# Optimization experiments

Measured on AMD Instinct MI355X. Metric: run time of the kernel, lower is better.

## Reference

```python
import jax, jax.numpy as jnp
import numpy as np

EPS = 1e-5  # torch BatchNorm default


def setup_inputs() -> dict:
    key = jax.random.key(0)
    k1, k2, k3 = jax.random.split(key, 3)
    N, C, T, V, O = 64, 64, 300, 25, 64
    x = jax.random.normal(k1, (N, C, T, V), dtype=jnp.float32)
    # 24 = V-1 convs, each (O, C, 1, 2) -> packed as (V-1, O, C, 2), scaled like conv_init
    W = jax.random.normal(k2, (V - 1, O, C, 2), dtype=jnp.float32) * (1.0 / np.sqrt(2 * C))
    b = jax.random.normal(k3, (V - 1, O), dtype=jnp.float32) * 0.01
    gamma = jnp.ones((O,), dtype=jnp.float32)
    beta = jnp.zeros((O,), dtype=jnp.float32)
    return {"x": x, "W": W, "b": b, "gamma": gamma, "beta": beta}


def reference(x, W, b, gamma, beta):
    # x: (N, C, T, V); W: (V-1, O, C, 2); b: (V-1, O)
    # Math of the original loop: out[..., v] = sum_i W0_i @ x[..., v]
    #   + sum_i W1_i @ x[..., (v+i+1) % V] + sum_i b_i
    V = x.shape[-1]
    W0 = W[..., 0]  # (V-1, O, C)
    W1 = W[..., 1]  # (V-1, O, C)
    # identity-tap term: all W0 share the same column -> sum once
    S0 = W0.sum(axis=0)  # (O, C)
    out = jnp.einsum('oc,nctv->notv', S0, x)
    # circular term: source u = (v+i+1)%V  <=>  i = (u-v-1)%V, valid for u != v
    v_idx = jnp.arange(V)
    off = (v_idx[None, :] - v_idx[:, None] - 1) % V  # (V_target, V_source) -> i, equals V-1 when u==v
    W1p = jnp.concatenate([W1, jnp.zeros_like(W1[:1])], axis=0)  # index V-1 maps to zero (u==v excluded)
    Wg = W1p[off]  # (V, V, O, C), zero on the diagonal
    out = out + jnp.einsum('vuoc,nctu->notv', Wg, x)
    out = out + b.sum(axis=0)[None, :, None, None]
    # BatchNorm2d (training-mode batch stats, biased variance) + ReLU
    mean = out.mean(axis=(0, 2, 3), keepdims=True)
    var = out.var(axis=(0, 2, 3), keepdims=True)
    out = (out - mean) * jax.lax.rsqrt(var + EPS)
    out = out * gamma[None, :, None, None] + beta[None, :, None, None]
    return jax.nn.relu(out)
```

## Files before the change

kernel.cpp:

```cpp
#include <hip/hip_runtime.h>


typedef short  s16x8 __attribute__((ext_vector_type(8)));
typedef float  f32x4 __attribute__((ext_vector_type(4)));

#define T_      300
#define TB_     19
#define NTHR_   320
#define ASTRIDE 136
#define TSTR    404

__device__ __forceinline__ unsigned short f2bf(float f) {
  unsigned u = __builtin_bit_cast(unsigned, f);
  return (unsigned short)((u + 0x7FFFu + ((u >> 16) & 1u)) >> 16);
}

__global__ void pack_w_kernel(const float* __restrict__ W, s16x8* __restrict__ Wg) {
  int idx = blockIdx.x * 256 + threadIdx.x;
  if (idx >= 12800) return;
  int lane  = idx & 63;
  int ni    = (idx >> 6) & 3;
  int chunk = (idx >> 8) & 1;
  int s     = idx >> 9;
  int o     = (ni << 4) + (lane & 15);
  int cbase = (chunk << 5) + ((lane >> 4) << 3);
  s16x8 h;
#pragma unroll
  for (int j = 0; j < 8; ++j) {
    int c = cbase + j;
    float val;
    if (s == 0) {
      val = 0.f;
      for (int i = 0; i < 24; ++i) val += W[((i * 64 + o) * 64 + c) * 2];
    } else {
      val = W[(((s - 1) * 64 + o) * 64 + c) * 2 + 1];
    }
    h[j] = (short)f2bf(val);
  }
  Wg[idx] = h;
}

__global__ __launch_bounds__(NTHR_) void tap_mm_kernel(
    const float* __restrict__ x, const s16x8* __restrict__ Wg,
    float* __restrict__ out, float* __restrict__ partials) {
  __shared__ __align__(16) char Ash[54400];
  __shared__ float red2[640];
  int n  = blockIdx.x;
  int tb = blockIdx.y;
  int t0 = tb * 16;
  int validRows = min(16, T_ - t0) * 25;
  int tid = threadIdx.x;
  const float* xn = x + n * 480000 + t0 * 25;

#pragma unroll 5
  for (int it = 0; it < 10; ++it) {
    int id  = tid + it * NTHR_;
    int pos = id % 400;
    int g   = id / 400;
    bool vld = pos < validRows;
    s16x8 h;
#pragma unroll
    for (int j = 0; j < 8; ++j) {
      float f = vld ? xn[((g << 3) + j) * 7500 + pos] : 0.f;
      h[j] = (short)f2bf(f);
    }
    *(s16x8*)(Ash + pos * ASTRIDE + (g << 4)) = h;
  }

  int wid = tid >> 6, lane = tid & 63;
  int l15 = lane & 15, lk = lane >> 4;
  int u[5], ao[5];
#pragma unroll
  for (int r = 0; r < 5; ++r) {
    int orow = ((wid * 5 + r) << 4) + l15;
    int tL = orow / 25;
    u[r]  = orow - tL * 25;
    ao[r] = orow * ASTRIDE + (lk << 4);
  }
  f32x4 acc[5][4];
#pragma unroll
  for (int r = 0; r < 5; ++r)
#pragma unroll
    for (int ct = 0; ct < 4; ++ct) acc[r][ct] = (f32x4){0.f, 0.f, 0.f, 0.f};

  s16x8 bf0[4], bf1[4];
#pragma unroll
  for (int ni = 0; ni < 4; ++ni) bf0[ni] = Wg[(ni << 6) + lane];
#pragma unroll
  for (int ni = 0; ni < 4; ++ni) bf1[ni] = Wg[256 + (ni << 6) + lane];

  __syncthreads();

  s16x8 afc = *(const s16x8*)(Ash + ao[0]);

  for (int s = 0; s < 25; ++s) {
    int snx = (s == 24) ? 0 : s + 1;
    const s16x8* wq0 = Wg + ((snx << 1) << 8);
    const s16x8* wq1 = wq0 + 256;
    __builtin_amdgcn_s_setprio(1);
#pragma unroll
    for (int r = 0; r < 5; ++r) {
      s16x8 nx = *(const s16x8*)(Ash + ((r < 4) ? ao[r + 1] : ao[0] + 64));
      acc[r][0] = __builtin_amdgcn_mfma_f32_16x16x32_bf16(afc, bf0[0], acc[r][0], 0, 0, 0);
      acc[r][1] = __builtin_amdgcn_mfma_f32_16x16x32_bf16(afc, bf0[1], acc[r][1], 0, 0, 0);
      acc[r][2] = __builtin_amdgcn_mfma_f32_16x16x32_bf16(afc, bf0[2], acc[r][2], 0, 0, 0);
      acc[r][3] = __builtin_amdgcn_mfma_f32_16x16x32_bf16(afc, bf0[3], acc[r][3], 0, 0, 0);
      afc = nx;
    }
    __builtin_amdgcn_s_setprio(0);
#pragma unroll
    for (int ni = 0; ni < 4; ++ni) bf0[ni] = wq0[(ni << 6) + lane];
    __builtin_amdgcn_s_setprio(1);
#pragma unroll
    for (int r = 0; r < 5; ++r) {
      int na;
      if (r < 4) {
        na = ao[r + 1] + 64;
      } else {
#pragma unroll
        for (int rr = 0; rr < 5; ++rr) {
          bool w = (u[rr] == 24);
          u[rr]  = w ? 0 : u[rr] + 1;
          ao[rr] += w ? -(24 * ASTRIDE) : ASTRIDE;
        }
        na = ao[0];
      }
      s16x8 nx = *(const s16x8*)(Ash + na);
      acc[r][0] = __builtin_amdgcn_mfma_f32_16x16x32_bf16(afc, bf1[0], acc[r][0], 0, 0, 0);
      acc[r][1] = __builtin_amdgcn_mfma_f32_16x16x32_bf16(afc, bf1[1], acc[r][1], 0, 0, 0);
      acc[r][2] = __builtin_amdgcn_mfma_f32_16x16x32_bf16(afc, bf1[2], acc[r][2], 0, 0, 0);
      acc[r][3] = __builtin_amdgcn_mfma_f32_16x16x32_bf16(afc, bf1[3], acc[r][3], 0, 0, 0);
      afc = nx;
    }
    __builtin_amdgcn_s_setprio(0);
#pragma unroll
    for (int ni = 0; ni < 4; ++ni) bf1[ni] = wq1[(ni << 6) + lane];
  }

  float s1v[4] = {0.f, 0.f, 0.f, 0.f}, s2v[4] = {0.f, 0.f, 0.f, 0.f};
#pragma unroll
  for (int r = 0; r < 5; ++r) {
#pragma unroll
    for (int qq = 0; qq < 4; ++qq) {
      int orow = ((wid * 5 + r) << 4) + (lk << 2) + qq;
      if (orow < validRows) {
#pragma unroll
        for (int ct = 0; ct < 4; ++ct) {
          float val = acc[r][ct][qq];
          s1v[ct] += val;
          s2v[ct] += val * val;
        }
      }
    }
  }
#pragma unroll
  for (int ct = 0; ct < 4; ++ct) {
    float a = s1v[ct], b = s2v[ct];
    a += __shfl_xor(a, 16); a += __shfl_xor(a, 32);
    b += __shfl_xor(b, 16); b += __shfl_xor(b, 32);
    if (lane < 16) {
      int base = ((((wid << 2) + ct) << 4) + l15) * 2;
      red2[base]     = a;
      red2[base + 1] = b;
    }
  }

  float* T = (float*)Ash;
  float* outb = out + n * 480000 + tb * 400;
  for (int qt = 0; qt < 4; ++qt) {
    __syncthreads();
#pragma unroll
    for (int r = 0; r < 5; ++r) {
      int row0 = wid * 80 + r * 16 + (lk << 2);
      *(f32x4*)&T[l15 * TSTR + row0] = acc[r][qt];
    }
    __syncthreads();
    if (qt == 0 && tid < 128) {
      int o = tid >> 1, m = tid & 1;
      int ct = o >> 4, ol = o & 15;
      float sres = 0.f;
#pragma unroll
      for (int w = 0; w < 5; ++w) sres += red2[((((w << 2) + ct) << 4) + ol) * 2 + m];
      int bl = blockIdx.y * 64 + blockIdx.x;
      partials[bl * 128 + m * 64 + o] = sres;
    }
#pragma unroll
    for (int i = 0; i < 5; ++i) {
      int idx = tid + i * 320;
      int ol  = idx / 100;
      int r4  = idx - ol * 100;
      if ((r4 << 2) < validRows) {
        float4 v = *(float4*)&T[ol * TSTR + (r4 << 2)];
        *(float4*)&outb[((qt << 4) + ol) * 7500 + (r4 << 2)] = v;
      }
    }
  }
}

__global__ void finalize_kernel(const float* __restrict__ part,
                                const float* __restrict__ gamma,
                                const float* __restrict__ beta,
                                float* __restrict__ scsh) {
  __shared__ float sm[512];
  int o = blockIdx.x;
  int tid = threadIdx.x;
  float s1 = 0.f, s2 = 0.f;
  for (int b = tid; b < 1216; b += 256) {
    s1 += part[b * 128 + o];
    s2 += part[b * 128 + 64 + o];
  }
  sm[tid] = s1; sm[256 + tid] = s2;
  __syncthreads();
  for (int st = 128; st >= 1; st >>= 1) {
    if (tid < st) { sm[tid] += sm[tid + st]; sm[256 + tid] += sm[256 + tid + st]; }
    __syncthreads();
  }
  if (tid == 0) {
    const float inv = 1.0f / 480000.0f;
    float mean = sm[0] * inv;
    float var  = sm[256] * inv - mean * mean;
    float sc = gamma[o] * rsqrtf(var + 1e-5f);
    float sh = beta[o] - mean * sc;
    scsh[o]      = sc;
    scsh[64 + o] = sh;
  }
}

__global__ void bn_relu_kernel(float4* __restrict__ out, const float* __restrict__ scsh) {
  int i = blockIdx.x * blockDim.x + threadIdx.x;
  const int total = 7680000;
  int stride = gridDim.x * blockDim.x;
  for (; i < total; i += stride) {
    int o = (i / 1875) & 63;
    float sc = scsh[o], sh = scsh[64 + o];
    float4 v = out[i];
    v.x = fmaxf(fmaf(v.x, sc, sh), 0.f);
    v.y = fmaxf(fmaf(v.y, sc, sh), 0.f);
    v.z = fmaxf(fmaf(v.z, sc, sh), 0.f);
    v.w = fmaxf(fmaf(v.w, sc, sh), 0.f);
    out[i] = v;
  }
}

extern "C" void kernel_launch(void* const* d_in, const int* in_sizes, int n_in,
                              void* d_out, int out_size, void* d_ws, size_t ws_size,
                              hipStream_t stream) {
  const float* x     = (const float*)d_in[0];
  const float* W     = (const float*)d_in[1];
  const float* gamma = (const float*)d_in[3];
  const float* beta  = (const float*)d_in[4];
  float* out = (float*)d_out;

  char* ws = (char*)d_ws;
  s16x8* Wg       = (s16x8*)ws;
  float* partials = (float*)(ws + 204800);
  float* scsh     = (float*)(ws + 204800 + 622592);

  pack_w_kernel<<<dim3(50), dim3(256), 0, stream>>>(W, Wg);
  tap_mm_kernel<<<dim3(64, TB_), dim3(NTHR_), 0, stream>>>(x, Wg, out, partials);
  finalize_kernel<<<dim3(64), dim3(256), 0, stream>>>(partials, gamma, beta, scsh);
  bn_relu_kernel<<<dim3(2048), dim3(256), 0, stream>>>((float4*)out, scsh);
}
```

Measured before the change: 212.6 us.

## Double-buffer weight fragments two taps ahead and keep per-row A fragments in registers

Restructures the tap loop so weight fragments for two taps are held in two register sets (A/B), prefetching each set two taps ahead instead of one, and keeps five A-row fragments resident so each MFMA group loads its next fragment right after use. It also widens the LDS row stride from 136 to 144 bytes and drops the setprio hints. The aim is to hide global weight-load latency and LDS latency behind more MFMA work, at the cost of higher VGPR usage and a different LDS bank pattern.

New measurement: 208.0 us. -2.1%, faster.

```diff
diff --git a/kernel.cpp b/kernel.cpp
--- a/kernel.cpp
+++ b/kernel.cpp
@@ -7,7 +7,7 @@
 #define T_      300
 #define TB_     19
 #define NTHR_   320
-#define ASTRIDE 136
+#define ASTR    144
 #define TSTR    404
 
 __device__ __forceinline__ unsigned short f2bf(float f) {
@@ -40,10 +40,39 @@
   Wg[idx] = h;
 }
 
+#define MF(J, Q0, Q1, Q2, Q3, SR)                                               \
+  acc[J][0] = __builtin_amdgcn_mfma_f32_16x16x32_bf16(SR, Q0, acc[J][0], 0, 0, 0); \
+  acc[J][1] = __builtin_amdgcn_mfma_f32_16x16x32_bf16(SR, Q1, acc[J][1], 0, 0, 0); \
+  acc[J][2] = __builtin_amdgcn_mfma_f32_16x16x32_bf16(SR, Q2, acc[J][2], 0, 0, 0); \
+  acc[J][3] = __builtin_amdgcn_mfma_f32_16x16x32_bf16(SR, Q3, acc[J][3], 0, 0, 0);
+
+#define ADV(J)                                                                  \
+  { bool w_ = (u[J] == 24); u[J] = w_ ? 0 : u[J] + 1;                           \
+    ao[J] += w_ ? -(24 * ASTR) : ASTR; }
+
+#define PHASE(BA0, BA1, BA2, BA3, BA4, BA5, BA6, BA7, SN)                       \
+  {                                                                             \
+    const s16x8* wq_ = Wg + (SN) * 512;                                         \
+    MF(0, BA0, BA1, BA2, BA3, S0) S0 = *(const s16x8*)(Ash + ao[0] + 64);       \
+    MF(1, BA0, BA1, BA2, BA3, S1) S1 = *(const s16x8*)(Ash + ao[1] + 64);       \
+    MF(2, BA0, BA1, BA2, BA3, S2) S2 = *(const s16x8*)(Ash + ao[2] + 64);       \
+    MF(3, BA0, BA1, BA2, BA3, S3) S3 = *(const s16x8*)(Ash + ao[3] + 64);       \
+    MF(4, BA0, BA1, BA2, BA3, S4) S4 = *(const s16x8*)(Ash + ao[4] + 64);       \
+    BA0 = wq_[lane];       BA1 = wq_[64 + lane];                                \
+    BA2 = wq_[128 + lane]; BA3 = wq_[192 + lane];                               \
+    ADV(0) MF(0, BA4, BA5, BA6, BA7, S0) S0 = *(const s16x8*)(Ash + ao[0]);     \
+    ADV(1) MF(1, BA4, BA5, BA6, BA7, S1) S1 = *(const s16x8*)(Ash + ao[1]);     \
+    ADV(2) MF(2, BA4, BA5, BA6, BA7, S2) S2 = *(const s16x8*)(Ash + ao[2]);     \
+    ADV(3) MF(3, BA4, BA5, BA6, BA7, S3) S3 = *(const s16x8*)(Ash + ao[3]);     \
+    ADV(4) MF(4, BA4, BA5, BA6, BA7, S4) S4 = *(const s16x8*)(Ash + ao[4]);     \
+    BA4 = wq_[256 + lane]; BA5 = wq_[320 + lane];                               \
+    BA6 = wq_[384 + lane]; BA7 = wq_[448 + lane];                               \
+  }
+
 __global__ __launch_bounds__(NTHR_) void tap_mm_kernel(
     const float* __restrict__ x, const s16x8* __restrict__ Wg,
     float* __restrict__ out, float* __restrict__ partials) {
-  __shared__ __align__(16) char Ash[54400];
+  __shared__ __align__(16) char Ash[57600];
   __shared__ float red2[640];
   int n  = blockIdx.x;
   int tb = blockIdx.y;
@@ -52,6 +81,18 @@
   int tid = threadIdx.x;
   const float* xn = x + n * 480000 + t0 * 25;
 
+  int wid = tid >> 6, lane = tid & 63;
+  int l15 = lane & 15, lk = lane >> 4;
+
+  s16x8 bfA0 = Wg[lane],       bfA1 = Wg[64 + lane];
+  s16x8 bfA2 = Wg[128 + lane], bfA3 = Wg[192 + lane];
+  s16x8 bfA4 = Wg[256 + lane], bfA5 = Wg[320 + lane];
+  s16x8 bfA6 = Wg[384 + lane], bfA7 = Wg[448 + lane];
+  s16x8 bfB0 = Wg[512 + lane], bfB1 = Wg[576 + lane];
+  s16x8 bfB2 = Wg[640 + lane], bfB3 = Wg[704 + lane];
+  s16x8 bfB4 = Wg[768 + lane], bfB5 = Wg[832 + lane];
+  s16x8 bfB6 = Wg[896 + lane], bfB7 = Wg[960 + lane];
+
 #pragma unroll 5
   for (int it = 0; it < 10; ++it) {
     int id  = tid + it * NTHR_;
@@ -64,18 +105,16 @@
       float f = vld ? xn[((g << 3) + j) * 7500 + pos] : 0.f;
       h[j] = (short)f2bf(f);
     }
-    *(s16x8*)(Ash + pos * ASTRIDE + (g << 4)) = h;
-  }
-
-  int wid = tid >> 6, lane = tid & 63;
-  int l15 = lane & 15, lk = lane >> 4;
+    *(s16x8*)(Ash + pos * ASTR + (g << 4)) = h;
+  }
+
   int u[5], ao[5];
 #pragma unroll
   for (int r = 0; r < 5; ++r) {
     int orow = ((wid * 5 + r) << 4) + l15;
     int tL = orow / 25;
     u[r]  = orow - tL * 25;
-    ao[r] = orow * ASTRIDE + (lk << 4);
+    ao[r] = orow * ASTR + (lk << 4);
   }
   f32x4 acc[5][4];
 #pragma unroll
@@ -83,59 +122,21 @@
 #pragma unroll
     for (int ct = 0; ct < 4; ++ct) acc[r][ct] = (f32x4){0.f, 0.f, 0.f, 0.f};
 
-  s16x8 bf0[4], bf1[4];
-#pragma unroll
-  for (int ni = 0; ni < 4; ++ni) bf0[ni] = Wg[(ni << 6) + lane];
-#pragma unroll
-  for (int ni = 0; ni < 4; ++ni) bf1[ni] = Wg[256 + (ni << 6) + lane];
-
   __syncthreads();
 
-  s16x8 afc = *(const s16x8*)(Ash + ao[0]);
-
-  for (int s = 0; s < 25; ++s) {
-    int snx = (s == 24) ? 0 : s + 1;
-    const s16x8* wq0 = Wg + ((snx << 1) << 8);
-    const s16x8* wq1 = wq0 + 256;
-    __builtin_amdgcn_s_setprio(1);
-#pragma unroll
-    for (int r = 0; r < 5; ++r) {
-      s16x8 nx = *(const s16x8*)(Ash + ((r < 4) ? ao[r + 1] : ao[0] + 64));
-      acc[r][0] = __builtin_amdgcn_mfma_f32_16x16x32_bf16(afc, bf0[0], acc[r][0], 0, 0, 0);
-      acc[r][1] = __builtin_amdgcn_mfma_f32_16x16x32_bf16(afc, bf0[1], acc[r][1], 0, 0, 0);
-      acc[r][2] = __builtin_amdgcn_mfma_f32_16x16x32_bf16(afc, bf0[2], acc[r][2], 0, 0, 0);
-      acc[r][3] = __builtin_amdgcn_mfma_f32_16x16x32_bf16(afc, bf0[3], acc[r][3], 0, 0, 0);
-      afc = nx;
-    }
-    __builtin_amdgcn_s_setprio(0);
-#pragma unroll
-    for (int ni = 0; ni < 4; ++ni) bf0[ni] = wq0[(ni << 6) + lane];
-    __builtin_amdgcn_s_setprio(1);
-#pragma unroll
-    for (int r = 0; r < 5; ++r) {
-      int na;
-      if (r < 4) {
-        na = ao[r + 1] + 64;
-      } else {
-#pragma unroll
-        for (int rr = 0; rr < 5; ++rr) {
-          bool w = (u[rr] == 24);
-          u[rr]  = w ? 0 : u[rr] + 1;
-          ao[rr] += w ? -(24 * ASTRIDE) : ASTRIDE;
-        }
-        na = ao[0];
-      }
-      s16x8 nx = *(const s16x8*)(Ash + na);
-      acc[r][0] = __builtin_amdgcn_mfma_f32_16x16x32_bf16(afc, bf1[0], acc[r][0], 0, 0, 0);
-      acc[r][1] = __builtin_amdgcn_mfma_f32_16x16x32_bf16(afc, bf1[1], acc[r][1], 0, 0, 0);
-      acc[r][2] = __builtin_amdgcn_mfma_f32_16x16x32_bf16(afc, bf1[2], acc[r][2], 0, 0, 0);
-      acc[r][3] = __builtin_amdgcn_mfma_f32_16x16x32_bf16(afc, bf1[3], acc[r][3], 0, 0, 0);
-      afc = nx;
-    }
-    __builtin_amdgcn_s_setprio(0);
-#pragma unroll
-    for (int ni = 0; ni < 4; ++ni) bf1[ni] = wq1[(ni << 6) + lane];
-  }
+  s16x8 S0 = *(const s16x8*)(Ash + ao[0]);
+  s16x8 S1 = *(const s16x8*)(Ash + ao[1]);
+  s16x8 S2 = *(const s16x8*)(Ash + ao[2]);
+  s16x8 S3 = *(const s16x8*)(Ash + ao[3]);
+  s16x8 S4 = *(const s16x8*)(Ash + ao[4]);
+
+  for (int k = 0; k < 12; ++k) {
+    int sA = 2 * k + 2;
+    int sB = 2 * k + 3; sB -= (sB >= 25) ? 25 : 0;
+    PHASE(bfA0, bfA1, bfA2, bfA3, bfA4, bfA5, bfA6, bfA7, sA)
+    PHASE(bfB0, bfB1, bfB2, bfB3, bfB4, bfB5, bfB6, bfB7, sB)
+  }
+  PHASE(bfA0, bfA1, bfA2, bfA3, bfA4, bfA5, bfA6, bfA7, 1)
 
   float s1v[4] = {0.f, 0.f, 0.f, 0.f}, s2v[4] = {0.f, 0.f, 0.f, 0.f};
 #pragma unroll
```
